# Optimization experiments

Measured on AMD Instinct MI355X. Metric: run time of the kernel, lower is better.

Reference implementation:

```python
import jax, jax.numpy as jnp
import numpy as np

NUM_HEADS = 16
NEG = -10000000.0


def setup_inputs() -> dict:
    key = jax.random.key(0)
    k1, k2, k3 = jax.random.split(key, 3)
    B, N, C = 4, 2048, 1024
    inputs = jax.random.normal(k1, (B, N, C), dtype=jnp.float32)
    # learned params (xavier-ish scale)
    W_qkv = jax.random.normal(k2, (C, 3 * C), dtype=jnp.float32) * 0.02
    W_proj = jax.random.normal(k3, (C, C), dtype=jnp.float32) * 0.02
    b_proj = jnp.zeros((C,), dtype=jnp.float32)
    attn_mask = jnp.ones((N, N), dtype=jnp.int32)      # >0 means keep
    padding_mask = jnp.zeros((B, N), dtype=jnp.int32)  # >0 means mask out
    return {"inputs": inputs, "attn_mask": attn_mask, "padding_mask": padding_mask,
            "W_qkv": W_qkv, "W_proj": W_proj, "b_proj": b_proj}


def reference(inputs, attn_mask, padding_mask, W_qkv, W_proj, b_proj):
    B, N, C = inputs.shape
    H = NUM_HEADS
    d = C // H
    scale = d ** -0.5
    qkv = inputs @ W_qkv                                   # [B,N,3C]
    qkv = qkv.reshape(B, N, 3, H, d).transpose(2, 0, 3, 1, 4)  # [3,B,H,N,d]
    q, k, v = qkv[0], qkv[1], qkv[2]
    scores = jnp.einsum('bhqd,bhkd->bhqk', q, k) * scale   # [B,H,N,N]
    scores = jnp.where(attn_mask > 0, scores, NEG)
    pm = padding_mask[:, None, None, :]                    # [B,1,1,N]
    scores = jnp.where(pm > 0, NEG, scores)
    attn = jax.nn.softmax(scores, axis=-1)
    x = jnp.einsum('bhqk,bhkd->bhqd', attn, v)             # [B,H,N,d]
    x = x.swapaxes(1, 2).reshape(B, N, C)
    return x @ W_proj + b_proj
```

## Files before the change

kernel.cpp:

```cpp
#include <hip/hip_runtime.h>

#define NEG -10000000.0f
#define QSCALE 0.18033688011112042f

typedef __attribute__((ext_vector_type(8))) short bf16x8;
typedef __attribute__((ext_vector_type(4))) float f32x4;

static __device__ __forceinline__ short f2bf(float f) {
    unsigned int u = __float_as_uint(f);
    unsigned int r = (u + 0x7fffu + ((u >> 16) & 1u)) >> 16;
    return (short)r;
}

static __device__ __forceinline__ unsigned pack_bf16_2(float a, float b) {
    unsigned ua = __float_as_uint(a) + 0x8000u;
    unsigned ub = __float_as_uint(b) + 0x8000u;
    return __builtin_amdgcn_perm(ub, ua, 0x07060302u);
}

static __device__ __forceinline__ void async_cp16(const void* g, void* l) {
    __builtin_amdgcn_global_load_lds(
        (const __attribute__((address_space(1))) unsigned int*)g,
        (__attribute__((address_space(3))) unsigned int*)l, 16, 0, 0);
}

__global__ void cvt_bf16(const float* __restrict__ src, short* __restrict__ dst, int n4) {
    int i = blockIdx.x * blockDim.x + threadIdx.x;
    if (i < n4) {
        float4 v = reinterpret_cast<const float4*>(src)[i];
        short4 o;
        o.x = f2bf(v.x); o.y = f2bf(v.y); o.z = f2bf(v.z); o.w = f2bf(v.w);
        reinterpret_cast<short4*>(dst)[i] = o;
    }
}

__global__ void transpose_cvt(const float* __restrict__ src, short* __restrict__ dst,
                              int rows, int cols) {
    __shared__ float tile[32][33];
    int bx = blockIdx.x * 32;
    int by = blockIdx.y * 32;
    int tx = threadIdx.x & 31, ty = threadIdx.x >> 5;
    for (int j = 0; j < 4; ++j)
        tile[ty + j * 8][tx] = src[(size_t)(by + ty + j * 8) * cols + bx + tx];
    __syncthreads();
    for (int j = 0; j < 4; ++j)
        dst[(size_t)(bx + ty + j * 8) * rows + by + tx] = f2bf(tile[tx][ty + j * 8]);
}

__global__ void mask_flags(const int* __restrict__ attn_mask, int* __restrict__ flags) {
    int blk = blockIdx.x;
    int qt = blk >> 5, kt = blk & 31;
    int tid = threadIdx.x;
    __shared__ int blockok;
    if (tid == 0) blockok = 1;
    __syncthreads();
    int ok = 1;
    for (int j = 0; j < 32; ++j) {
        int idx = j * 256 + tid;
        int qr = qt * 128 + (idx >> 6);
        int kc = kt * 64 + (idx & 63);
        ok &= (attn_mask[(size_t)qr * 2048 + kc] != 0);
    }
    if (!ok) blockok = 0;
    __syncthreads();
    if (tid == 0) flags[blk] = blockok;
}

__global__ void pad_flags(const int* __restrict__ padding, int* __restrict__ pf) {
    int t = threadIdx.x;
    int b = t >> 5, kt = t & 31;
    int any = 0;
    for (int j = 0; j < 64; ++j) any |= (padding[b * 2048 + kt * 64 + j] > 0);
    pf[t] = any;
}

__global__ __launch_bounds__(256, 2) void gemm_bf16(
    const short* __restrict__ A, const short* __restrict__ Bt, int mode,
    short* __restrict__ q_ws, short* __restrict__ k_ws, short* __restrict__ v_ws,
    float* __restrict__ out, const float* __restrict__ bias) {
    const int K = 1024;
    __shared__ __align__(16) short smem[2][128][64];
    short (*As)[64] = smem[0];
    short (*Bs)[64] = smem[1];
    int tid = threadIdx.x, lane = tid & 63, w = tid >> 6;
    int wm = w & 1, wn = w >> 1;
    int m0 = blockIdx.y * 128, n0 = blockIdx.x * 128;
    int col = lane & 15, quad = lane >> 4;
    int l8 = lane >> 3, j8 = lane & 7;

    f32x4 acc[4][4] = {};

    for (int k0 = 0; k0 < K; k0 += 64) {
        for (int c = 0; c < 4; ++c) {
            int rr = w * 32 + c * 8 + l8;
            int sw = (j8 ^ (rr & 7)) << 3;
            async_cp16(&A[(size_t)(m0 + rr) * K + k0 + sw], &As[w * 32 + c * 8][0]);
            async_cp16(&Bt[(size_t)(n0 + rr) * K + k0 + sw], &Bs[w * 32 + c * 8][0]);
        }
        __syncthreads();
        for (int ks = 0; ks < 2; ++ks) {
            bf16x8 af[4], bfr[4];
            for (int mt = 0; mt < 4; ++mt)
                af[mt] = *reinterpret_cast<const bf16x8*>(
                    &As[wm * 64 + mt * 16 + col][((ks * 4 + quad) ^ (col & 7)) << 3]);
            for (int nt = 0; nt < 4; ++nt)
                bfr[nt] = *reinterpret_cast<const bf16x8*>(
                    &Bs[wn * 64 + nt * 16 + col][((ks * 4 + quad) ^ (col & 7)) << 3]);
            for (int mt = 0; mt < 4; ++mt)
                for (int nt = 0; nt < 4; ++nt)
                    acc[mt][nt] = __builtin_amdgcn_mfma_f32_16x16x32_bf16(af[mt], bfr[nt], acc[mt][nt], 0, 0, 0);
        }
        __syncthreads();
    }

    short* L = &smem[0][0][0];

    if (mode == 0) {
        int which = n0 >> 10;
        int cb = n0 & 1023;
        int b = m0 >> 11, nb = m0 & 2047, hb = cb >> 6;
        if (which == 2) {
            for (int mt = 0; mt < 4; ++mt)
                for (int nt = 0; nt < 4; ++nt) {
                    int ml = wm * 64 + mt * 16 + quad * 4;
                    int cl = wn * 64 + nt * 16 + col;
                    int mp = (ml + 8 * cl) & 127;
                    short4 pk;
                    for (int r = 0; r < 4; ++r) ((short*)&pk)[r] = f2bf(acc[mt][nt][r]);
                    *reinterpret_cast<short4*>(&L[cl * 128 + mp]) = pk;
                }
            __syncthreads();
            for (int it = 0; it < 8; ++it) {
                int chunk = it * 256 + tid;
                int c = chunk >> 4, j = chunk & 15;
                int h = hb + (c >> 6), dd = c & 63;
                int4 val = *reinterpret_cast<const int4*>(&L[c * 128 + (((j + c) & 15) << 3)]);
                *reinterpret_cast<int4*>(
                    &v_ws[((size_t)((b * 16 + h) * 64 + dd)) * 2048 + nb + j * 8]) = val;
            }
        } else {
            short* dst = (which == 0) ? q_ws : k_ws;
            float scl = (which == 0) ? QSCALE : 1.0f;
            for (int mt = 0; mt < 4; ++mt)
                for (int nt = 0; nt < 4; ++nt)
                    for (int r = 0; r < 4; ++r) {
                        int ml = wm * 64 + mt * 16 + quad * 4 + r;
                        int cl = wn * 64 + nt * 16 + col;
                        L[ml * 128 + ((cl + 8 * ml) & 127)] = f2bf(acc[mt][nt][r] * scl);
                    }
            __syncthreads();
            for (int it = 0; it < 8; ++it) {
                int chunk = it * 256 + tid;
                int row = chunk >> 4, j = chunk & 15;
                int h = hb + (j >> 3), dd = (j & 7) * 8;
                int4 val = *reinterpret_cast<const int4*>(&L[row * 128 + (((j + row) & 15) << 3)]);
                *reinterpret_cast<int4*>(
                    &dst[((size_t)(b * 16 + h) * 2048 + nb + row) * 64 + dd]) = val;
            }
        }
    } else {
        float* Lf = reinterpret_cast<float*>(L);
        for (int half = 0; half < 2; ++half) {
            if (wm == half) {
                for (int mt = 0; mt < 4; ++mt)
                    for (int nt = 0; nt < 4; ++nt)
                        for (int r = 0; r < 4; ++r) {
                            int ml = mt * 16 + quad * 4 + r;
                            int cl = wn * 64 + nt * 16 + col;
                            Lf[ml * 128 + cl] = acc[mt][nt][r];
                        }
            }
            __syncthreads();
            for (int it = 0; it < 8; ++it) {
                int chunk = it * 256 + tid;
                int row = chunk >> 5, j = chunk & 31;
                float4 val = *reinterpret_cast<const float4*>(&Lf[row * 128 + j * 4]);
                float4 bv = *reinterpret_cast<const float4*>(&bias[n0 + j * 4]);
                val.x += bv.x; val.y += bv.y; val.z += bv.z; val.w += bv.w;
                *reinterpret_cast<float4*>(
                    &out[(size_t)(m0 + half * 64 + row) * 1024 + n0 + j * 4]) = val;
            }
            __syncthreads();
        }
    }
}

__global__ __launch_bounds__(256, 4) void flash_attn(
    const short* __restrict__ q_ws, const short* __restrict__ k_ws,
    const short* __restrict__ v_ws, const int* __restrict__ aflags,
    const int* __restrict__ pflags, const int* __restrict__ padding,
    const int* __restrict__ attn_mask, short* __restrict__ xb) {
    const int Nn = 2048, D = 64;
    __shared__ short QP[128][64];
    __shared__ short Ks[64][64];
    __shared__ short Vt[64][64];
    __shared__ __align__(16) float padb[64];

    int tid = threadIdx.x, lane = tid & 63, w = tid >> 6;
    int col = lane & 15, quad = lane >> 4;
    int bh = blockIdx.y, b = bh >> 4, h = bh & 15;
    int q0 = blockIdx.x * 128, qt = blockIdx.x;
    int l8 = lane >> 3, j8 = lane & 7;

    for (int c = 0; c < 4; ++c) {
        int rr = w * 32 + c * 8 + l8;
        async_cp16(&q_ws[((size_t)bh * Nn + q0 + rr) * D + ((j8 ^ (rr & 7)) << 3)],
                   &QP[w * 32 + c * 8][0]);
    }
    __syncthreads();

    bf16x8 qf[2][2];
    for (int t = 0; t < 2; ++t)
        for (int ks = 0; ks < 2; ++ks)
            qf[t][ks] = *reinterpret_cast<const bf16x8*>(
                &QP[w * 32 + t * 16 + col][((ks * 4 + quad) ^ (col & 7)) << 3]);

    f32x4 oacc[2][4] = {};
    f32x4 lacc[2] = {};

    for (int kt = 0; kt < 32; ++kt) {
        int k0 = kt * 64;
        for (int c = 0; c < 2; ++c) {
            int rr = w * 16 + c * 8 + l8;
            int sw = (j8 ^ (rr & 7)) << 3;
            async_cp16(&k_ws[((size_t)bh * Nn + k0 + rr) * D + sw], &Ks[w * 16 + c * 8][0]);
            async_cp16(&v_ws[((size_t)bh * D + rr) * Nn + k0 + sw], &Vt[w * 16 + c * 8][0]);
        }
        int pflag = pflags[b * 32 + kt];
        if (pflag && tid < 64) padb[tid] = (padding[b * Nn + k0 + tid] > 0) ? NEG : 0.f;
        __syncthreads();

        f32x4 sacc[4][2] = {};
        for (int ks = 0; ks < 2; ++ks) {
            bf16x8 kf[4];
            for (int mt = 0; mt < 4; ++mt)
                kf[mt] = *reinterpret_cast<const bf16x8*>(
                    &Ks[mt * 16 + col][((ks * 4 + quad) ^ (col & 7)) << 3]);
            for (int mt = 0; mt < 4; ++mt)
                for (int t = 0; t < 2; ++t)
                    sacc[mt][t] = __builtin_amdgcn_mfma_f32_16x16x32_bf16(kf[mt], qf[t][ks], sacc[mt][t], 0, 0, 0);
        }

        if (!aflags[qt * 32 + kt]) {
            for (int mt = 0; mt < 4; ++mt)
                for (int t = 0; t < 2; ++t)
                    for (int r = 0; r < 4; ++r) {
                        int kc = k0 + mt * 16 + quad * 4 + r;
                        int qr = q0 + w * 32 + t * 16 + col;
                        if (attn_mask[(size_t)qr * Nn + kc] == 0) sacc[mt][t][r] = NEG;
                    }
        }
        if (pflag) {
            for (int mt = 0; mt < 4; ++mt) {
                f32x4 pb = *reinterpret_cast<const f32x4*>(&padb[mt * 16 + quad * 4]);
                for (int t = 0; t < 2; ++t)
                    for (int r = 0; r < 4; ++r) sacc[mt][t][r] += pb[r];
            }
        }

        for (int t = 0; t < 2; ++t) {
            int qrow = w * 32 + t * 16 + col;
            for (int mt = 0; mt < 4; ++mt) {
                f32x4 e;
                e[0] = __builtin_amdgcn_exp2f(sacc[mt][t][0]);
                e[1] = __builtin_amdgcn_exp2f(sacc[mt][t][1]);
                e[2] = __builtin_amdgcn_exp2f(sacc[mt][t][2]);
                e[3] = __builtin_amdgcn_exp2f(sacc[mt][t][3]);
                lacc[t] += e;
                unsigned p0 = pack_bf16_2(e[0], e[1]);
                unsigned p1 = pack_bf16_2(e[2], e[3]);
                int chunk = (mt * 2 + (quad >> 1)) ^ (col & 7);
                *reinterpret_cast<uint2*>(&QP[qrow][(chunk << 3) + ((quad & 1) << 2)]) =
                    make_uint2(p0, p1);
            }
        }

        for (int ks = 0; ks < 2; ++ks) {
            bf16x8 pf[2], vf[4];
            for (int t = 0; t < 2; ++t)
                pf[t] = *reinterpret_cast<const bf16x8*>(
                    &QP[w * 32 + t * 16 + col][((ks * 4 + quad) ^ (col & 7)) << 3]);
            for (int nt = 0; nt < 4; ++nt)
                vf[nt] = *reinterpret_cast<const bf16x8*>(
                    &Vt[nt * 16 + col][((ks * 4 + quad) ^ (col & 7)) << 3]);
            for (int t = 0; t < 2; ++t)
                for (int nt = 0; nt < 4; ++nt)
                    oacc[t][nt] = __builtin_amdgcn_mfma_f32_16x16x32_bf16(pf[t], vf[nt], oacc[t][nt], 0, 0, 0);
        }
        __syncthreads();
    }

    for (int t = 0; t < 2; ++t) {
        float ls = lacc[t][0] + lacc[t][1] + lacc[t][2] + lacc[t][3];
        ls += __shfl_xor(ls, 16);
        ls += __shfl_xor(ls, 32);
        for (int r = 0; r < 4; ++r) {
            float lv = __shfl(ls, quad * 4 + r, 16);
            float inv = 1.f / lv;
            int n = q0 + w * 32 + t * 16 + quad * 4 + r;
            for (int nt = 0; nt < 4; ++nt) {
                int dd = nt * 16 + col;
                xb[((size_t)(b * Nn + n)) * 1024 + h * 64 + dd] = f2bf(oacc[t][nt][r] * inv);
            }
        }
    }
}

extern "C" void kernel_launch(void* const* d_in, const int* in_sizes, int n_in,
                              void* d_out, int out_size, void* d_ws, size_t ws_size,
                              hipStream_t stream) {
    const float* x        = (const float*)d_in[0];
    const int* attn_mask  = (const int*)d_in[1];
    const int* padding    = (const int*)d_in[2];
    const float* W_qkv    = (const float*)d_in[3];
    const float* W_proj   = (const float*)d_in[4];
    const float* b_proj   = (const float*)d_in[5];
    float* out            = (float*)d_out;

    char* ws = (char*)d_ws;
    short* Xb   = (short*)(ws);
    short* Wqt  = (short*)(ws + (16u << 20));
    short* Wpt  = (short*)(ws + (22u << 20));
    short* q_ws = (short*)(ws + (24u << 20));
    short* k_ws = (short*)(ws + (40u << 20));
    short* v_ws = (short*)(ws + (56u << 20));
    short* xbuf = (short*)(ws + (72u << 20));
    int*  flags = (int*)(ws + (88u << 20));

    cvt_bf16<<<8192, 256, 0, stream>>>(x, Xb, 8388608 / 4);
    transpose_cvt<<<dim3(3072 / 32, 1024 / 32), 256, 0, stream>>>(W_qkv, Wqt, 1024, 3072);
    transpose_cvt<<<dim3(1024 / 32, 1024 / 32), 256, 0, stream>>>(W_proj, Wpt, 1024, 1024);
    mask_flags<<<512, 256, 0, stream>>>(attn_mask, flags);
    pad_flags<<<1, 128, 0, stream>>>(padding, flags + 512);

    gemm_bf16<<<dim3(3072 / 128, 8192 / 128), 256, 0, stream>>>(
        Xb, Wqt, 0, q_ws, k_ws, v_ws, nullptr, nullptr);

    flash_attn<<<dim3(16, 64), 256, 0, stream>>>(
        q_ws, k_ws, v_ws, flags, flags + 512, padding, attn_mask, xbuf);

    gemm_bf16<<<dim3(1024 / 128, 8192 / 128), 256, 0, stream>>>(
        xbuf, Wpt, 1, nullptr, nullptr, nullptr, out, b_proj);
}
```

Measured before the change: 287.2 us.

## Double-buffer K/V tiles and software-pipeline QK^T one tile ahead in flash attention

Flash attention now double-buffers the K and V shared-memory tiles and issues async global-to-LDS loads for later tiles while the current one is processed. The QK^T MFMAs for the next tile are computed before the PV MFMAs of the current tile, so score computation overlaps with softmax and PV work, and there is one barrier per iteration instead of two. The padding bias is read straight from global memory instead of staging through LDS. In exchange it uses more LDS and registers, and launch bounds drop from 4 to 3 blocks per CU.

```diff
diff --git a/kernel.cpp b/kernel.cpp
--- a/kernel.cpp
+++ b/kernel.cpp
@@ -118,7 +118,7 @@
     if (mode == 0) {
         int which = n0 >> 10;
         int cb = n0 & 1023;
-        int b = m0 >> 11, nb = m0 & 2047, hb = cb >> 6;
+        int b = m0 >> 11, nbase = m0 & 2047, hb = cb >> 6;
         if (which == 2) {
             for (int mt = 0; mt < 4; ++mt)
                 for (int nt = 0; nt < 4; ++nt) {
@@ -136,7 +136,7 @@
                 int h = hb + (c >> 6), dd = c & 63;
                 int4 val = *reinterpret_cast<const int4*>(&L[c * 128 + (((j + c) & 15) << 3)]);
                 *reinterpret_cast<int4*>(
-                    &v_ws[((size_t)((b * 16 + h) * 64 + dd)) * 2048 + nb + j * 8]) = val;
+                    &v_ws[((size_t)((b * 16 + h) * 64 + dd)) * 2048 + nbase + j * 8]) = val;
             }
         } else {
             short* dst = (which == 0) ? q_ws : k_ws;
@@ -155,7 +155,7 @@
                 int h = hb + (j >> 3), dd = (j & 7) * 8;
                 int4 val = *reinterpret_cast<const int4*>(&L[row * 128 + (((j + row) & 15) << 3)]);
                 *reinterpret_cast<int4*>(
-                    &dst[((size_t)(b * 16 + h) * 2048 + nb + row) * 64 + dd]) = val;
+                    &dst[((size_t)(b * 16 + h) * 2048 + nbase + row) * 64 + dd]) = val;
             }
         }
     } else {
@@ -185,28 +185,39 @@
     }
 }
 
-__global__ __launch_bounds__(256, 4) void flash_attn(
+__global__ __launch_bounds__(256, 3) void flash_attn(
     const short* __restrict__ q_ws, const short* __restrict__ k_ws,
     const short* __restrict__ v_ws, const int* __restrict__ aflags,
     const int* __restrict__ pflags, const int* __restrict__ padding,
     const int* __restrict__ attn_mask, short* __restrict__ xb) {
     const int Nn = 2048, D = 64;
     __shared__ short QP[128][64];
-    __shared__ short Ks[64][64];
-    __shared__ short Vt[64][64];
-    __shared__ __align__(16) float padb[64];
+    __shared__ short Ks[2][64][64];
+    __shared__ short Vt[2][64][64];
 
     int tid = threadIdx.x, lane = tid & 63, w = tid >> 6;
     int col = lane & 15, quad = lane >> 4;
     int bh = blockIdx.y, b = bh >> 4, h = bh & 15;
     int q0 = blockIdx.x * 128, qt = blockIdx.x;
     int l8 = lane >> 3, j8 = lane & 7;
-
-    for (int c = 0; c < 4; ++c) {
-        int rr = w * 32 + c * 8 + l8;
-        async_cp16(&q_ws[((size_t)bh * Nn + q0 + rr) * D + ((j8 ^ (rr & 7)) << 3)],
-                   &QP[w * 32 + c * 8][0]);
-    }
+    int swz = (j8 ^ l8) << 3;
+
+    const short* kgw = k_ws + ((size_t)bh * Nn + w * 16 + l8) * D + swz;
+    const short* vgw = v_ws + ((size_t)bh * D + w * 16 + l8) * Nn + swz;
+
+    {
+        const short* qg = q_ws + ((size_t)bh * Nn + q0 + w * 32 + l8) * D + swz;
+        async_cp16(qg,          &QP[w * 32][0]);
+        async_cp16(qg + 8 * D,  &QP[w * 32 + 8][0]);
+        async_cp16(qg + 16 * D, &QP[w * 32 + 16][0]);
+        async_cp16(qg + 24 * D, &QP[w * 32 + 24][0]);
+    }
+    async_cp16(kgw,              &Ks[0][w * 16][0]);
+    async_cp16(kgw + 8 * D,      &Ks[0][w * 16 + 8][0]);
+    async_cp16(kgw + 64 * D,     &Ks[1][w * 16][0]);
+    async_cp16(kgw + 72 * D,     &Ks[1][w * 16 + 8][0]);
+    async_cp16(vgw,              &Vt[0][w * 16][0]);
+    async_cp16(vgw + 8 * Nn,     &Vt[0][w * 16 + 8][0]);
     __syncthreads();
 
     bf16x8 qf[2][2];
@@ -217,28 +228,30 @@
 
     f32x4 oacc[2][4] = {};
     f32x4 lacc[2] = {};
-
-    for (int kt = 0; kt < 32; ++kt) {
+    f32x4 sA[4][2] = {}, sB[4][2] = {};
+
+    for (int ks = 0; ks < 2; ++ks)
+        for (int mt = 0; mt < 4; ++mt) {
+            bf16x8 kf = *reinterpret_cast<const bf16x8*>(
+                &Ks[0][mt * 16 + col][((ks * 4 + quad) ^ (col & 7)) << 3]);
+            sA[mt][0] = __builtin_amdgcn_mfma_f32_16x16x32_bf16(kf, qf[0][ks], sA[mt][0], 0, 0, 0);
+            sA[mt][1] = __builtin_amdgcn_mfma_f32_16x16x32_bf16(kf, qf[1][ks], sA[mt][1], 0, 0, 0);
+        }
+    __syncthreads();
+
+    auto iter_body = [&](int kt, f32x4 (&scur)[4][2], f32x4 (&snxt)[4][2]) {
+        int cur = kt & 1;
         int k0 = kt * 64;
-        for (int c = 0; c < 2; ++c) {
-            int rr = w * 16 + c * 8 + l8;
-            int sw = (j8 ^ (rr & 7)) << 3;
-            async_cp16(&k_ws[((size_t)bh * Nn + k0 + rr) * D + sw], &Ks[w * 16 + c * 8][0]);
-            async_cp16(&v_ws[((size_t)bh * D + rr) * Nn + k0 + sw], &Vt[w * 16 + c * 8][0]);
-        }
-        int pflag = pflags[b * 32 + kt];
-        if (pflag && tid < 64) padb[tid] = (padding[b * Nn + k0 + tid] > 0) ? NEG : 0.f;
-        __syncthreads();
-
-        f32x4 sacc[4][2] = {};
-        for (int ks = 0; ks < 2; ++ks) {
-            bf16x8 kf[4];
-            for (int mt = 0; mt < 4; ++mt)
-                kf[mt] = *reinterpret_cast<const bf16x8*>(
-                    &Ks[mt * 16 + col][((ks * 4 + quad) ^ (col & 7)) << 3]);
-            for (int mt = 0; mt < 4; ++mt)
-                for (int t = 0; t < 2; ++t)
-                    sacc[mt][t] = __builtin_amdgcn_mfma_f32_16x16x32_bf16(kf[mt], qf[t][ks], sacc[mt][t], 0, 0, 0);
+
+        if (kt < 30) {
+            const short* kn = kgw + (size_t)(kt + 2) * 64 * D;
+            async_cp16(kn,         &Ks[cur][w * 16][0]);
+            async_cp16(kn + 8 * D, &Ks[cur][w * 16 + 8][0]);
+        }
+        if (kt < 31) {
+            const short* vn = vgw + (kt + 1) * 64;
+            async_cp16(vn,          &Vt[cur ^ 1][w * 16][0]);
+            async_cp16(vn + 8 * Nn, &Vt[cur ^ 1][w * 16 + 8][0]);
         }
 
         if (!aflags[qt * 32 + kt]) {
@@ -247,14 +260,17 @@
                     for (int r = 0; r < 4; ++r) {
                         int kc = k0 + mt * 16 + quad * 4 + r;
                         int qr = q0 + w * 32 + t * 16 + col;
-                        if (attn_mask[(size_t)qr * Nn + kc] == 0) sacc[mt][t][r] = NEG;
+                        if (attn_mask[(size_t)qr * Nn + kc] == 0) scur[mt][t][r] = NEG;
                     }
         }
-        if (pflag) {
+        if (pflags[b * 32 + kt]) {
             for (int mt = 0; mt < 4; ++mt) {
-                f32x4 pb = *reinterpret_cast<const f32x4*>(&padb[mt * 16 + quad * 4]);
+                int4 pv = *reinterpret_cast<const int4*>(&padding[b * Nn + k0 + mt * 16 + quad * 4]);
+                f32x4 pb;
+                pb[0] = (pv.x > 0) ? NEG : 0.f; pb[1] = (pv.y > 0) ? NEG : 0.f;
+                pb[2] = (pv.z > 0) ? NEG : 0.f; pb[3] = (pv.w > 0) ? NEG : 0.f;
                 for (int t = 0; t < 2; ++t)
-                    for (int r = 0; r < 4; ++r) sacc[mt][t][r] += pb[r];
+                    for (int r = 0; r < 4; ++r) scur[mt][t][r] += pb[r];
             }
         }
 
@@ -262,10 +278,10 @@
             int qrow = w * 32 + t * 16 + col;
             for (int mt = 0; mt < 4; ++mt) {
                 f32x4 e;
-                e[0] = __builtin_amdgcn_exp2f(sacc[mt][t][0]);
-                e[1] = __builtin_amdgcn_exp2f(sacc[mt][t][1]);
-                e[2] = __builtin_amdgcn_exp2f(sacc[mt][t][2]);
-                e[3] = __builtin_amdgcn_exp2f(sacc[mt][t][3]);
+                e[0] = __builtin_amdgcn_exp2f(scur[mt][t][0]);
+                e[1] = __builtin_amdgcn_exp2f(scur[mt][t][1]);
+                e[2] = __builtin_amdgcn_exp2f(scur[mt][t][2]);
+                e[3] = __builtin_amdgcn_exp2f(scur[mt][t][3]);
                 lacc[t] += e;
                 unsigned p0 = pack_bf16_2(e[0], e[1]);
                 unsigned p1 = pack_bf16_2(e[2], e[3]);
@@ -273,6 +289,18 @@
                 *reinterpret_cast<uint2*>(&QP[qrow][(chunk << 3) + ((quad & 1) << 2)]) =
                     make_uint2(p0, p1);
             }
+        }
+
+        if (kt < 31) {
+            for (int mt = 0; mt < 4; ++mt)
+                for (int t = 0; t < 2; ++t) snxt[mt][t] = {};
+            for (int ks = 0; ks < 2; ++ks)
+                for (int mt = 0; mt < 4; ++mt) {
+                    bf16x8 kf = *reinterpret_cast<const bf16x8*>(
+                        &Ks[cur ^ 1][mt * 16 + col][((ks * 4 + quad) ^ (col & 7)) << 3]);
+                    snxt[mt][0] = __builtin_amdgcn_mfma_f32_16x16x32_bf16(kf, qf[0][ks], snxt[mt][0], 0, 0, 0);
+                    snxt[mt][1] = __builtin_amdgcn_mfma_f32_16x16x32_bf16(kf, qf[1][ks], snxt[mt][1], 0, 0, 0);
+                }
         }
 
         for (int ks = 0; ks < 2; ++ks) {
@@ -282,12 +310,18 @@
                     &QP[w * 32 + t * 16 + col][((ks * 4 + quad) ^ (col & 7)) << 3]);
             for (int nt = 0; nt < 4; ++nt)
                 vf[nt] = *reinterpret_cast<const bf16x8*>(
-                    &Vt[nt * 16 + col][((ks * 4 + quad) ^ (col & 7)) << 3]);
+                    &Vt[cur][nt * 16 + col][((ks * 4 + quad) ^ (col & 7)) << 3]);
             for (int t = 0; t < 2; ++t)
                 for (int nt = 0; nt < 4; ++nt)
                     oacc[t][nt] = __builtin_amdgcn_mfma_f32_16x16x32_bf16(pf[t], vf[nt], oacc[t][nt], 0, 0, 0);
         }
+
         __syncthreads();
+    };
+
+    for (int kt = 0; kt < 32; kt += 2) {
+        iter_body(kt, sA, sB);
+        iter_body(kt + 1, sB, sA);
     }
 
     for (int t = 0; t < 2; ++t) {
```

Result: slower. 503.4 us (+75.2%).
